# Performance work log

Hardware: AMD Instinct MI355X
Metric: run time of the kernel (lower is better)

The kernel has to match this reference:

```python
import jax, jax.numpy as jnp
import numpy as np

T, H, I, E, TOP_K = 2048, 1024, 768, 8, 2


def setup_inputs() -> dict:
    key = jax.random.key(0)
    kx, kg, ku, kd, kr = jax.random.split(key, 5)
    scale_h = 1.0 / np.sqrt(H)
    scale_i = 1.0 / np.sqrt(I)
    x = jax.random.normal(kx, (T, H), dtype=jnp.float32)
    gate_w = jax.random.normal(kg, (E, I, H), dtype=jnp.float32) * scale_h
    up_w = jax.random.normal(ku, (E, I, H), dtype=jnp.float32) * scale_h
    down_w = jax.random.normal(kd, (E, H, I), dtype=jnp.float32) * scale_i
    # Router: top-k over random logits, softmax over selected, scatter to dense [T, E]
    logits = jax.random.normal(kr, (T, E), dtype=jnp.float32)
    top_vals, top_idx = jax.lax.top_k(logits, TOP_K)          # [T, K]
    top_w = jax.nn.softmax(top_vals, axis=-1)                 # [T, K]
    rows = jnp.arange(T)[:, None]                             # [T, 1]
    masked_routing_weights = jnp.zeros((T, E), jnp.float32).at[rows, top_idx].set(top_w)
    expert_select_count = jnp.zeros((E,), jnp.int32).at[top_idx.reshape(-1)].add(1)
    return {
        "x": x,
        "gate_w": gate_w,
        "up_w": up_w,
        "down_w": down_w,
        "masked_routing_weights": masked_routing_weights,
        "expert_select_count": expert_select_count,
    }


def reference(x, gate_w, up_w, down_w, masked_routing_weights, expert_select_count):
    # custom_moe_glu: per-expert GLU MLP, combined with masked routing weights.
    # x: [T, H]; gate_w/up_w: [E, I, H]; down_w: [E, H, I]; routing: [T, E]
    g = jnp.einsum("th,eih->tei", x, gate_w)                  # [T, E, I]
    u = jnp.einsum("th,eih->tei", x, up_w)                    # [T, E, I]
    h = jax.nn.silu(g) * u                                    # fused GLU activation
    # down projection per expert, then weighted combine over experts
    out = jnp.einsum("tei,ehi,te->th", h, down_w, masked_routing_weights)
    return out
```

## Files before the change

### kernel.cpp

```cpp
#include <hip/hip_runtime.h>
#include <hip/hip_bf16.h>

#define T_TOK 2048
#define H_DIM 1024
#define I_DIM 768
#define NEXP  8
#define WPE   6291456

typedef short bf16x8  __attribute__((ext_vector_type(8)));
typedef short short4v __attribute__((ext_vector_type(4)));
typedef float f32x4   __attribute__((ext_vector_type(4)));

__device__ __forceinline__ short f2bf(float f) {
  __bf16 b = (__bf16)f;
  return __builtin_bit_cast(short, b);
}
__device__ __forceinline__ void gload16(const void* g, void* l) {
  __builtin_amdgcn_global_load_lds(
      (const __attribute__((address_space(1))) void*)g,
      (__attribute__((address_space(3))) void*)l, 16, 0, 0);
}
__device__ __forceinline__ int padcnt(int c) { return (c + 127) & ~127; }
__device__ __forceinline__ int ebase(const int* __restrict__ cnts, int e) {
  int b = 0;
#pragma unroll
  for (int i = 0; i < NEXP; ++i)
    if (i < e) b += padcnt(cnts[i]);
  return b;
}


__global__ __launch_bounds__(512) void compact_k(const float* __restrict__ routw,
                                                 int* __restrict__ wsI) {
  __shared__ int sc[8];
  int e = blockIdx.x, lane = threadIdx.x & 63, w = threadIdx.x >> 6;
  unsigned long long mk[4];
  int cnt = 0;
#pragma unroll
  for (int c = 0; c < 4; ++c) {
    int tk = w * 256 + c * 64 + lane;
    float v = routw[(size_t)tk * NEXP + e];
    mk[c] = __ballot(v > 0.f);
    cnt += __popcll(mk[c]);
  }
  if (lane == 0) sc[w] = cnt;
  __syncthreads();
  int run = 0;
#pragma unroll
  for (int j = 0; j < 8; ++j)
    if (j < w) run += sc[j];
#pragma unroll
  for (int c = 0; c < 4; ++c) {
    int tk = w * 256 + c * 64 + lane;
    if ((mk[c] >> lane) & 1ull) {
      int pos = __popcll(mk[c] & ((1ull << lane) - 1));
      wsI[64 + e * T_TOK + run + pos] = tk;
    }
    run += __popcll(mk[c]);
  }
  if (w == 7 && lane == 0) wsI[e] = run;
}

__global__ __launch_bounds__(256) void pre_k(const float* __restrict__ x,
                                             const float* __restrict__ gw,
                                             const float* __restrict__ uw,
                                             const float* __restrict__ dw,
                                             const int* __restrict__ wsI,
                                             unsigned short* __restrict__ xc,
                                             unsigned short* __restrict__ wbf,
                                             float* __restrict__ out) {
  int bid = blockIdx.x, tid = threadIdx.x;
  if (bid < 4096) {
    int e = bid >> 9, rb = bid & 511;
    int cnt = wsI[e];
    int pad = padcnt(cnt);
    int r = rb * 4 + (tid >> 6);
    if (r >= pad) return;
    int base = ebase(wsI, e);
    int col = (tid & 63) * 16;
    unsigned short* dst = xc + (size_t)(base + r) * H_DIM + col;
    if (r < cnt) {
      int tok = wsI[64 + e * T_TOK + r];
      const float* sr = x + (size_t)tok * H_DIM + col;
#pragma unroll
      for (int j = 0; j < 4; ++j) {
        float4 v = *(const float4*)(sr + j * 4);
        short4v b = {f2bf(v.x), f2bf(v.y), f2bf(v.z), f2bf(v.w)};
        *(short4v*)(dst + j * 4) = b;
      }
    } else {
#pragma unroll
      for (int j = 0; j < 4; ++j) {
        short4v z = {0, 0, 0, 0};
        *(short4v*)(dst + j * 4) = z;
      }
    }
  } else if (bid < 8704) {
    size_t off = ((size_t)(bid - 4096) * 256 + tid) * 16;
    int a = (int)(off / (size_t)WPE);
    size_t rem = off - (size_t)a * WPE;
    const float* s = ((a == 0) ? gw : (a == 1) ? uw : dw) + rem;
    unsigned short* o = wbf + (size_t)a * WPE + rem;
#pragma unroll
    for (int j = 0; j < 4; ++j) {
      float4 v = *(const float4*)(s + j * 4);
      short4v b = {f2bf(v.x), f2bf(v.y), f2bf(v.z), f2bf(v.w)};
      *(short4v*)(o + j * 4) = b;
    }
  } else {
    size_t off = ((size_t)(bid - 8704) * 256 + tid) * 16;
    f32x4 z = {0.f, 0.f, 0.f, 0.f};
#pragma unroll
    for (int j = 0; j < 4; ++j) *(f32x4*)(out + off + j * 4) = z;
  }
}

#define WB(v)                                              \
  do {                                                     \
    asm volatile("s_waitcnt vmcnt(" #v ")" ::: "memory");  \
    __builtin_amdgcn_s_barrier();                          \
    __builtin_amdgcn_sched_barrier(0);                     \
  } while (0)

__global__ __launch_bounds__(512, 2) void gemm1_k(
    const unsigned short* __restrict__ xc, const unsigned short* __restrict__ wbf,
    const int* __restrict__ wsI, unsigned short* __restrict__ h) {
  int e = blockIdx.x & 7, rr = blockIdx.x >> 3;
  int mt = rr & 15, nt = rr >> 4;
  int cnt = wsI[e];
  int m0 = mt * 128;
  if (m0 >= cnt) return;
  int base = ebase(wsI, e);
  int n0 = nt * 128;

  __shared__ unsigned short ls[5][12288];

  int tid = threadIdx.x, lane = tid & 63, w = tid >> 6;
  int wm = w >> 2, wn = w & 3;
  int fr = lane & 15, fg = lane >> 4;
  int srow = lane >> 2;
  int scol = (((lane & 3) ^ (srow & 3) ^ ((srow >> 2) & 1))) * 8;

  const unsigned short* srcA = xc + (size_t)(base + m0 + 16 * w + srow) * H_DIM + scol;
  const unsigned short* srcG = wbf + (size_t)(e * I_DIM + n0 + 16 * w + srow) * H_DIM + scol;
  const unsigned short* srcU = wbf + WPE + (size_t)(e * I_DIM + n0 + 16 * w + srow) * H_DIM + scol;

  int sl = ((fg ^ (fr & 3) ^ ((fr >> 2) & 1)) << 3);
  int roA[4], roB[4];
#pragma unroll
  for (int m = 0; m < 4; ++m) roA[m] = (wm * 64 + m * 16 + fr) * 32 + sl;
#pragma unroll
  for (int n = 0; n < 4; ++n) {
    int r2 = (n < 2) ? (wn * 32 + n * 16 + fr) : (128 + wn * 32 + (n - 2) * 16 + fr);
    roB[n] = 4096 + r2 * 32 + sl;
  }

  bf16x8 af[2][4], bv[2][4];
  f32x4 acc[4][4] = {};

#define STG1(hh)                                                     \
  do {                                                               \
    unsigned short* lb = &ls[(hh) % 5][0];                           \
    gload16(srcA + (hh) * 32, lb + w * 512);                         \
    gload16(srcG + (hh) * 32, lb + 4096 + w * 512);                  \
    gload16(srcU + (hh) * 32, lb + 4096 + (w + 8) * 512);            \
  } while (0)
#define LDF1(st, hh)                                                 \
  do {                                                               \
    const unsigned short* lb = &ls[(hh) % 5][0];                     \
    _Pragma("unroll") for (int m = 0; m < 4; ++m) af[st][m] = *(const bf16x8*)(lb + roA[m]); \
    _Pragma("unroll") for (int n = 0; n < 4; ++n) bv[st][n] = *(const bf16x8*)(lb + roB[n]); \
  } while (0)
#define MM1(st)                                                      \
  do {                                                               \
    __builtin_amdgcn_s_setprio(1);                                   \
    _Pragma("unroll") for (int m = 0; m < 4; ++m)                    \
      _Pragma("unroll") for (int n = 0; n < 4; ++n)                  \
        acc[m][n] = __builtin_amdgcn_mfma_f32_16x16x32_bf16(af[st][m], bv[st][n], acc[m][n], 0, 0, 0); \
    __builtin_amdgcn_s_setprio(0);                                   \
  } while (0)

  STG1(0); STG1(1); STG1(2); STG1(3);
  WB(6);
  LDF1(0, 0);
#pragma unroll
  for (int i = 0; i < 32; ++i) {
    if (i + 4 < 32) STG1(i + 4);
    if (i + 1 < 32) LDF1((i + 1) & 1, i + 1);
    MM1(i & 1);
    if (i <= 27)      WB(6);
    else if (i == 28) WB(3);
    else if (i == 29) WB(0);
  }
#undef STG1
#undef LDF1
#undef MM1

#pragma unroll
  for (int m = 0; m < 4; ++m)
#pragma unroll
    for (int j = 0; j < 4; ++j) {
      int row = wm * 64 + m * 16 + fg * 4 + j;
      size_t rb2 = (size_t)(base + m0 + row) * I_DIM + n0;
#pragma unroll
      for (int jn = 0; jn < 2; ++jn) {
        float g = acc[m][jn][j];
        float u = acc[m][jn + 2][j];
        h[rb2 + wn * 32 + jn * 16 + fr] = (unsigned short)f2bf(g * u / (1.f + __expf(-g)));
      }
    }
}

__global__ __launch_bounds__(512, 2) void gemm2_k(
    const unsigned short* __restrict__ h, const unsigned short* __restrict__ wbf,
    const int* __restrict__ wsI, const float* __restrict__ routw,
    float* __restrict__ out) {
  int e = blockIdx.x & 7, rr = blockIdx.x >> 3;
  int mt = rr & 15, nt = rr >> 4;
  int cnt = wsI[e];
  int m0 = mt * 128;
  if (m0 >= cnt) return;
  int base = ebase(wsI, e);
  int n0 = nt * 256;
  const unsigned short* down_bf = wbf + 2 * (size_t)WPE;

  __shared__ unsigned short ls[5][12288];

  int tid = threadIdx.x, lane = tid & 63, w = tid >> 6;
  int wm = w >> 2, wn = w & 3;
  int fr = lane & 15, fg = lane >> 4;
  int srow = lane >> 2;
  int scol = (((lane & 3) ^ (srow & 3) ^ ((srow >> 2) & 1))) * 8;

  const unsigned short* srcA  = h + (size_t)(base + m0 + 16 * w + srow) * I_DIM + scol;
  const unsigned short* srcB1 = down_bf + (size_t)(e * H_DIM + n0 + 16 * w + srow) * I_DIM + scol;
  const unsigned short* srcB2 = down_bf + (size_t)(e * H_DIM + n0 + 16 * (w + 8) + srow) * I_DIM + scol;

  int sl = ((fg ^ (fr & 3) ^ ((fr >> 2) & 1)) << 3);
  int roA[4], roB[4];
#pragma unroll
  for (int m = 0; m < 4; ++m) roA[m] = (wm * 64 + m * 16 + fr) * 32 + sl;
#pragma unroll
  for (int n = 0; n < 4; ++n) roB[n] = 4096 + (wn * 64 + n * 16 + fr) * 32 + sl;

  bf16x8 af[2][4], bv[2][4];
  f32x4 acc[4][4] = {};

#define STG2(hh)                                                     \
  do {                                                               \
    unsigned short* lb = &ls[(hh) % 5][0];                           \
    gload16(srcA + (hh) * 32, lb + w * 512);                         \
    gload16(srcB1 + (hh) * 32, lb + 4096 + w * 512);                 \
    gload16(srcB2 + (hh) * 32, lb + 4096 + (w + 8) * 512);           \
  } while (0)
#define LDF2(st, hh)                                                 \
  do {                                                               \
    const unsigned short* lb = &ls[(hh) % 5][0];                     \
    _Pragma("unroll") for (int m = 0; m < 4; ++m) af[st][m] = *(const bf16x8*)(lb + roA[m]); \
    _Pragma("unroll") for (int n = 0; n < 4; ++n) bv[st][n] = *(const bf16x8*)(lb + roB[n]); \
  } while (0)
#define MM2(st)                                                      \
  do {                                                               \
    __builtin_amdgcn_s_setprio(1);                                   \
    _Pragma("unroll") for (int m = 0; m < 4; ++m)                    \
      _Pragma("unroll") for (int n = 0; n < 4; ++n)                  \
        acc[m][n] = __builtin_amdgcn_mfma_f32_16x16x32_bf16(af[st][m], bv[st][n], acc[m][n], 0, 0, 0); \
    __builtin_amdgcn_s_setprio(0);                                   \
  } while (0)

  STG2(0); STG2(1); STG2(2); STG2(3);
  WB(6);
  LDF2(0, 0);
#pragma unroll
  for (int i = 0; i < 24; ++i) {
    if (i + 4 < 24) STG2(i + 4);
    if (i + 1 < 24) LDF2((i + 1) & 1, i + 1);
    MM2(i & 1);
    if (i <= 19)      WB(6);
    else if (i == 20) WB(3);
    else if (i == 21) WB(0);
  }
#undef STG2
#undef LDF2
#undef MM2

#pragma unroll
  for (int m = 0; m < 4; ++m)
#pragma unroll
    for (int j = 0; j < 4; ++j) {
      int row = wm * 64 + m * 16 + fg * 4 + j;
      int grow = m0 + row;
      if (grow < cnt) {
        int tk = wsI[64 + e * T_TOK + grow];
        float rw = routw[(size_t)tk * NEXP + e];
        float* orow = out + (size_t)tk * H_DIM + n0 + wn * 64;
#pragma unroll
        for (int n = 0; n < 4; ++n)
          atomicAdd(orow + n * 16 + fr, acc[m][n][j] * rw);
      }
    }
}

extern "C" void kernel_launch(void* const* d_in, const int* in_sizes, int n_in,
                              void* d_out, int out_size, void* d_ws, size_t ws_size,
                              hipStream_t stream) {
  const float* x      = (const float*)d_in[0];
  const float* gate_w = (const float*)d_in[1];
  const float* up_w   = (const float*)d_in[2];
  const float* down_w = (const float*)d_in[3];
  const float* routw  = (const float*)d_in[4];
  float* out = (float*)d_out;
  int* wsI = (int*)d_ws;

  unsigned short* wbf = (unsigned short*)((char*)d_ws + 131072);
  unsigned short* xc  = (unsigned short*)((char*)d_ws + 37879808);
  unsigned short* h   = (unsigned short*)((char*)d_ws + 48365568);

  compact_k<<<8, 512, 0, stream>>>(routw, wsI);
  pre_k<<<9216, 256, 0, stream>>>(x, gate_w, up_w, down_w, wsI, xc, wbf, out);
  gemm1_k<<<768, 512, 0, stream>>>(xc, wbf, wsI, h);
  gemm2_k<<<512, 512, 0, stream>>>(h, wbf, wsI, routw, out);
}
```

Before: 93.52 us.

## Rewrite gate/up GEMM to load fragments directly from global, exchanging up via LDS

The first grouped GEMM drops its 5-stage LDS pipeline with async global-to-LDS loads. It now uses 256-thread blocks over 64-row tiles, where each wave loads its MFMA operands straight from global memory into registers with double buffering. Gate and up products are computed by separate waves, and the up results pass through a small padded LDS buffer so the gate waves can apply SiLU and write h. The intent is to cut LDS traffic and barriers and raise occupancy. The cost is that A and B tiles are no longer shared across waves, so global and L2 traffic per MFMA rises, and the uncoalesced 16-byte row loads may limit bandwidth.

Measured after the change: 151.0 us. 61.5% more time.

```diff
diff --git a/kernel.cpp b/kernel.cpp
--- a/kernel.cpp
+++ b/kernel.cpp
@@ -115,101 +115,96 @@
   }
 }
 
+__global__ __launch_bounds__(256, 3) void gemm1_k(
+    const unsigned short* __restrict__ xc, const unsigned short* __restrict__ wbf,
+    const int* __restrict__ wsI, unsigned short* __restrict__ h) {
+  int e = blockIdx.x & 7, rr = blockIdx.x >> 3;
+  int mt = rr & 31, ng = rr >> 5;
+  int cnt = wsI[e];
+  int m0 = mt * 64;
+  if (m0 >= cnt) return;
+  int base = ebase(wsI, e);
+
+  __shared__ float uex[2][64][65];
+
+  int tid = threadIdx.x, lane = tid & 63, w = tid >> 6;
+  int fr = lane & 15, fg = lane >> 4;
+  int isU = w >> 1;
+  int wp = w & 1;
+  int n0 = ng * 128 + 64 * wp;
+
+  const unsigned short* wsrc = wbf + (size_t)isU * WPE;
+  const unsigned short* pa[4];
+  const unsigned short* pb[4];
+#pragma unroll
+  for (int m = 0; m < 4; ++m)
+    pa[m] = xc + (size_t)(base + m0 + m * 16 + fr) * H_DIM + fg * 8;
+#pragma unroll
+  for (int n = 0; n < 4; ++n)
+    pb[n] = wsrc + (size_t)(e * I_DIM + n0 + n * 16 + fr) * H_DIM + fg * 8;
+
+  f32x4 acc[4][4] = {};
+  bf16x8 a0[4], b0[4], a1[4], b1[4];
+
+#define LD1(A, B, ks)                                                \
+  do {                                                               \
+    _Pragma("unroll") for (int m = 0; m < 4; ++m)                    \
+      A[m] = *(const bf16x8*)(pa[m] + (ks) * 32);                    \
+    _Pragma("unroll") for (int n = 0; n < 4; ++n)                    \
+      B[n] = *(const bf16x8*)(pb[n] + (ks) * 32);                    \
+  } while (0)
+#define MM1(A, B)                                                    \
+  do {                                                               \
+    _Pragma("unroll") for (int m = 0; m < 4; ++m)                    \
+      _Pragma("unroll") for (int n = 0; n < 4; ++n)                  \
+        acc[m][n] = __builtin_amdgcn_mfma_f32_16x16x32_bf16(A[m], B[n], acc[m][n], 0, 0, 0); \
+  } while (0)
+
+  LD1(a0, b0, 0);
+  LD1(a1, b1, 1);
+#pragma unroll
+  for (int i = 0; i < 16; ++i) {
+    MM1(a0, b0);
+    if (i < 15) LD1(a0, b0, 2 * i + 2);
+    MM1(a1, b1);
+    if (i < 15) LD1(a1, b1, 2 * i + 3);
+  }
+#undef LD1
+#undef MM1
+
+  if (isU) {
+#pragma unroll
+    for (int m = 0; m < 4; ++m)
+#pragma unroll
+      for (int n = 0; n < 4; ++n)
+#pragma unroll
+        for (int j = 0; j < 4; ++j)
+          uex[wp][m * 16 + fg * 4 + j][n * 16 + fr] = acc[m][n][j];
+  }
+  __syncthreads();
+  if (!isU) {
+#pragma unroll
+    for (int m = 0; m < 4; ++m)
+#pragma unroll
+      for (int j = 0; j < 4; ++j) {
+        int row = m * 16 + fg * 4 + j;
+        size_t hb = (size_t)(base + m0 + row) * I_DIM + n0;
+#pragma unroll
+        for (int n = 0; n < 4; ++n) {
+          float g = acc[m][n][j];
+          float u = uex[wp][row][n * 16 + fr];
+          h[hb + n * 16 + fr] = (unsigned short)f2bf(g * u / (1.f + __expf(-g)));
+        }
+      }
+  }
+}
+
 #define WB(v)                                              \
   do {                                                     \
     asm volatile("s_waitcnt vmcnt(" #v ")" ::: "memory");  \
     __builtin_amdgcn_s_barrier();                          \
     __builtin_amdgcn_sched_barrier(0);                     \
   } while (0)
-
-__global__ __launch_bounds__(512, 2) void gemm1_k(
-    const unsigned short* __restrict__ xc, const unsigned short* __restrict__ wbf,
-    const int* __restrict__ wsI, unsigned short* __restrict__ h) {
-  int e = blockIdx.x & 7, rr = blockIdx.x >> 3;
-  int mt = rr & 15, nt = rr >> 4;
-  int cnt = wsI[e];
-  int m0 = mt * 128;
-  if (m0 >= cnt) return;
-  int base = ebase(wsI, e);
-  int n0 = nt * 128;
-
-  __shared__ unsigned short ls[5][12288];
-
-  int tid = threadIdx.x, lane = tid & 63, w = tid >> 6;
-  int wm = w >> 2, wn = w & 3;
-  int fr = lane & 15, fg = lane >> 4;
-  int srow = lane >> 2;
-  int scol = (((lane & 3) ^ (srow & 3) ^ ((srow >> 2) & 1))) * 8;
-
-  const unsigned short* srcA = xc + (size_t)(base + m0 + 16 * w + srow) * H_DIM + scol;
-  const unsigned short* srcG = wbf + (size_t)(e * I_DIM + n0 + 16 * w + srow) * H_DIM + scol;
-  const unsigned short* srcU = wbf + WPE + (size_t)(e * I_DIM + n0 + 16 * w + srow) * H_DIM + scol;
-
-  int sl = ((fg ^ (fr & 3) ^ ((fr >> 2) & 1)) << 3);
-  int roA[4], roB[4];
-#pragma unroll
-  for (int m = 0; m < 4; ++m) roA[m] = (wm * 64 + m * 16 + fr) * 32 + sl;
-#pragma unroll
-  for (int n = 0; n < 4; ++n) {
-    int r2 = (n < 2) ? (wn * 32 + n * 16 + fr) : (128 + wn * 32 + (n - 2) * 16 + fr);
-    roB[n] = 4096 + r2 * 32 + sl;
-  }
-
-  bf16x8 af[2][4], bv[2][4];
-  f32x4 acc[4][4] = {};
-
-#define STG1(hh)                                                     \
-  do {                                                               \
-    unsigned short* lb = &ls[(hh) % 5][0];                           \
-    gload16(srcA + (hh) * 32, lb + w * 512);                         \
-    gload16(srcG + (hh) * 32, lb + 4096 + w * 512);                  \
-    gload16(srcU + (hh) * 32, lb + 4096 + (w + 8) * 512);            \
-  } while (0)
-#define LDF1(st, hh)                                                 \
-  do {                                                               \
-    const unsigned short* lb = &ls[(hh) % 5][0];                     \
-    _Pragma("unroll") for (int m = 0; m < 4; ++m) af[st][m] = *(const bf16x8*)(lb + roA[m]); \
-    _Pragma("unroll") for (int n = 0; n < 4; ++n) bv[st][n] = *(const bf16x8*)(lb + roB[n]); \
-  } while (0)
-#define MM1(st)                                                      \
-  do {                                                               \
-    __builtin_amdgcn_s_setprio(1);                                   \
-    _Pragma("unroll") for (int m = 0; m < 4; ++m)                    \
-      _Pragma("unroll") for (int n = 0; n < 4; ++n)                  \
-        acc[m][n] = __builtin_amdgcn_mfma_f32_16x16x32_bf16(af[st][m], bv[st][n], acc[m][n], 0, 0, 0); \
-    __builtin_amdgcn_s_setprio(0);                                   \
-  } while (0)
-
-  STG1(0); STG1(1); STG1(2); STG1(3);
-  WB(6);
-  LDF1(0, 0);
-#pragma unroll
-  for (int i = 0; i < 32; ++i) {
-    if (i + 4 < 32) STG1(i + 4);
-    if (i + 1 < 32) LDF1((i + 1) & 1, i + 1);
-    MM1(i & 1);
-    if (i <= 27)      WB(6);
-    else if (i == 28) WB(3);
-    else if (i == 29) WB(0);
-  }
-#undef STG1
-#undef LDF1
-#undef MM1
-
-#pragma unroll
-  for (int m = 0; m < 4; ++m)
-#pragma unroll
-    for (int j = 0; j < 4; ++j) {
-      int row = wm * 64 + m * 16 + fg * 4 + j;
-      size_t rb2 = (size_t)(base + m0 + row) * I_DIM + n0;
-#pragma unroll
-      for (int jn = 0; jn < 2; ++jn) {
-        float g = acc[m][jn][j];
-        float u = acc[m][jn + 2][j];
-        h[rb2 + wn * 32 + jn * 16 + fr] = (unsigned short)f2bf(g * u / (1.f + __expf(-g)));
-      }
-    }
-}
 
 __global__ __launch_bounds__(512, 2) void gemm2_k(
     const unsigned short* __restrict__ h, const unsigned short* __restrict__ wbf,
@@ -318,6 +313,6 @@
 
   compact_k<<<8, 512, 0, stream>>>(routw, wsI);
   pre_k<<<9216, 256, 0, stream>>>(x, gate_w, up_w, down_w, wsI, xc, wbf, out);
-  gemm1_k<<<768, 512, 0, stream>>>(xc, wbf, wsI, h);
+  gemm1_k<<<1536, 256, 0, stream>>>(xc, wbf, wsI, h);
   gemm2_k<<<512, 512, 0, stream>>>(h, wbf, wsI, routw, out);
 }
```

## Gather tokens inside gemm1 from padded bf16 x instead of precompacted copy

Applied to the files above, without the earlier changes.

Instead of building a per-expert compacted bf16 copy of x in the prep kernel, x is converted once into a bf16 buffer with an extra zero row, and gemm1 gathers rows by token index, with padding indices pointing at the zero row. The x and gate/up weight buffers also get a padded row stride of 1056 elements, likely to spread accesses across memory channels. This cuts prep-kernel traffic, since x is converted once rather than per expert assignment. The cost is an indirect, non-contiguous row load for the A operand in gemm1.

Result: faster. 91.60 us (-2.0%).

```diff
diff --git a/kernel.cpp b/kernel.cpp
--- a/kernel.cpp
+++ b/kernel.cpp
@@ -5,7 +5,8 @@
 #define H_DIM 1024
 #define I_DIM 768
 #define NEXP  8
-#define WPE   6291456
+#define XSTR  1056
+#define WSTR  1056
 
 typedef short bf16x8  __attribute__((ext_vector_type(8)));
 typedef short short4v __attribute__((ext_vector_type(4)));
@@ -33,7 +34,7 @@
 __global__ __launch_bounds__(512) void compact_k(const float* __restrict__ routw,
                                                  int* __restrict__ wsI) {
   __shared__ int sc[8];
-  int e = blockIdx.x, lane = threadIdx.x & 63, w = threadIdx.x >> 6;
+  int e = blockIdx.x, tid = threadIdx.x, lane = tid & 63, w = tid >> 6;
   unsigned long long mk[4];
   int cnt = 0;
 #pragma unroll
@@ -45,10 +46,12 @@
   }
   if (lane == 0) sc[w] = cnt;
   __syncthreads();
-  int run = 0;
-#pragma unroll
-  for (int j = 0; j < 8; ++j)
+  int run = 0, tot = 0;
+#pragma unroll
+  for (int j = 0; j < 8; ++j) {
     if (j < w) run += sc[j];
+    tot += sc[j];
+  }
 #pragma unroll
   for (int c = 0; c < 4; ++c) {
     int tk = w * 256 + c * 64 + lane;
@@ -58,30 +61,28 @@
     }
     run += __popcll(mk[c]);
   }
-  if (w == 7 && lane == 0) wsI[e] = run;
+  if (w == 7 && lane == 0) wsI[e] = tot;
+  int pad = padcnt(tot);
+  for (int r = tot + tid; r < pad; r += 512) wsI[64 + e * T_TOK + r] = T_TOK;
 }
 
 __global__ __launch_bounds__(256) void pre_k(const float* __restrict__ x,
                                              const float* __restrict__ gw,
                                              const float* __restrict__ uw,
                                              const float* __restrict__ dw,
-                                             const int* __restrict__ wsI,
-                                             unsigned short* __restrict__ xc,
-                                             unsigned short* __restrict__ wbf,
+                                             unsigned short* __restrict__ x_bf,
+                                             unsigned short* __restrict__ gbf,
+                                             unsigned short* __restrict__ ubf,
+                                             unsigned short* __restrict__ dbf,
                                              float* __restrict__ out) {
   int bid = blockIdx.x, tid = threadIdx.x;
-  if (bid < 4096) {
-    int e = bid >> 9, rb = bid & 511;
-    int cnt = wsI[e];
-    int pad = padcnt(cnt);
-    int r = rb * 4 + (tid >> 6);
-    if (r >= pad) return;
-    int base = ebase(wsI, e);
-    int col = (tid & 63) * 16;
-    unsigned short* dst = xc + (size_t)(base + r) * H_DIM + col;
-    if (r < cnt) {
-      int tok = wsI[64 + e * T_TOK + r];
-      const float* sr = x + (size_t)tok * H_DIM + col;
+  int col = (tid & 63) * 16;
+  if (bid < 520) {
+    int r = bid * 4 + (tid >> 6);
+    if (r > 2048) return;
+    unsigned short* dst = x_bf + (size_t)r * XSTR + col;
+    if (r < 2048) {
+      const float* sr = x + (size_t)r * H_DIM + col;
 #pragma unroll
       for (int j = 0; j < 4; ++j) {
         float4 v = *(const float4*)(sr + j * 4);
@@ -95,12 +96,21 @@
         *(short4v*)(dst + j * 4) = z;
       }
     }
-  } else if (bid < 8704) {
-    size_t off = ((size_t)(bid - 4096) * 256 + tid) * 16;
-    int a = (int)(off / (size_t)WPE);
-    size_t rem = off - (size_t)a * WPE;
-    const float* s = ((a == 0) ? gw : (a == 1) ? uw : dw) + rem;
-    unsigned short* o = wbf + (size_t)a * WPE + rem;
+  } else if (bid < 3592) {
+    int a = (bid < 2056) ? 0 : 1;
+    int r = (bid - (a ? 2056 : 520)) * 4 + (tid >> 6);
+    const float* s = (a ? uw : gw) + (size_t)r * H_DIM + col;
+    unsigned short* dst = (a ? ubf : gbf) + (size_t)r * WSTR + col;
+#pragma unroll
+    for (int j = 0; j < 4; ++j) {
+      float4 v = *(const float4*)(s + j * 4);
+      short4v b = {f2bf(v.x), f2bf(v.y), f2bf(v.z), f2bf(v.w)};
+      *(short4v*)(dst + j * 4) = b;
+    }
+  } else if (bid < 5128) {
+    size_t off = ((size_t)(bid - 3592) * 256 + tid) * 16;
+    const float* s = dw + off;
+    unsigned short* o = dbf + off;
 #pragma unroll
     for (int j = 0; j < 4; ++j) {
       float4 v = *(const float4*)(s + j * 4);
@@ -108,7 +118,7 @@
       *(short4v*)(o + j * 4) = b;
     }
   } else {
-    size_t off = ((size_t)(bid - 8704) * 256 + tid) * 16;
+    size_t off = ((size_t)(bid - 5128) * 256 + tid) * 16;
     f32x4 z = {0.f, 0.f, 0.f, 0.f};
 #pragma unroll
     for (int j = 0; j < 4; ++j) *(f32x4*)(out + off + j * 4) = z;
@@ -123,8 +133,9 @@
   } while (0)
 
 __global__ __launch_bounds__(512, 2) void gemm1_k(
-    const unsigned short* __restrict__ xc, const unsigned short* __restrict__ wbf,
-    const int* __restrict__ wsI, unsigned short* __restrict__ h) {
+    const unsigned short* __restrict__ x_bf, const unsigned short* __restrict__ gbf,
+    const unsigned short* __restrict__ ubf, const int* __restrict__ wsI,
+    unsigned short* __restrict__ h) {
   int e = blockIdx.x & 7, rr = blockIdx.x >> 3;
   int mt = rr & 15, nt = rr >> 4;
   int cnt = wsI[e];
@@ -141,9 +152,10 @@
   int srow = lane >> 2;
   int scol = (((lane & 3) ^ (srow & 3) ^ ((srow >> 2) & 1))) * 8;
 
-  const unsigned short* srcA = xc + (size_t)(base + m0 + 16 * w + srow) * H_DIM + scol;
-  const unsigned short* srcG = wbf + (size_t)(e * I_DIM + n0 + 16 * w + srow) * H_DIM + scol;
-  const unsigned short* srcU = wbf + WPE + (size_t)(e * I_DIM + n0 + 16 * w + srow) * H_DIM + scol;
+  int tokA = wsI[64 + e * T_TOK + m0 + 16 * w + srow];
+  const unsigned short* srcA = x_bf + (size_t)tokA * XSTR + scol;
+  const unsigned short* srcG = gbf + (size_t)(e * I_DIM + n0 + 16 * w + srow) * WSTR + scol;
+  const unsigned short* srcU = ubf + (size_t)(e * I_DIM + n0 + 16 * w + srow) * WSTR + scol;
 
   int sl = ((fg ^ (fr & 3) ^ ((fr >> 2) & 1)) << 3);
   int roA[4], roB[4];
@@ -212,7 +224,7 @@
 }
 
 __global__ __launch_bounds__(512, 2) void gemm2_k(
-    const unsigned short* __restrict__ h, const unsigned short* __restrict__ wbf,
+    const unsigned short* __restrict__ h, const unsigned short* __restrict__ dbf,
     const int* __restrict__ wsI, const float* __restrict__ routw,
     float* __restrict__ out) {
   int e = blockIdx.x & 7, rr = blockIdx.x >> 3;
@@ -222,7 +234,6 @@
   if (m0 >= cnt) return;
   int base = ebase(wsI, e);
   int n0 = nt * 256;
-  const unsigned short* down_bf = wbf + 2 * (size_t)WPE;
 
   __shared__ unsigned short ls[5][12288];
 
@@ -233,8 +244,8 @@
   int scol = (((lane & 3) ^ (srow & 3) ^ ((srow >> 2) & 1))) * 8;
 
   const unsigned short* srcA  = h + (size_t)(base + m0 + 16 * w + srow) * I_DIM + scol;
-  const unsigned short* srcB1 = down_bf + (size_t)(e * H_DIM + n0 + 16 * w + srow) * I_DIM + scol;
-  const unsigned short* srcB2 = down_bf + (size_t)(e * H_DIM + n0 + 16 * (w + 8) + srow) * I_DIM + scol;
+  const unsigned short* srcB1 = dbf + (size_t)(e * H_DIM + n0 + 16 * w + srow) * I_DIM + scol;
+  const unsigned short* srcB2 = dbf + (size_t)(e * H_DIM + n0 + 16 * (w + 8) + srow) * I_DIM + scol;
 
   int sl = ((fg ^ (fr & 3) ^ ((fr >> 2) & 1)) << 3);
   int roA[4], roB[4];
@@ -312,12 +323,14 @@
   float* out = (float*)d_out;
   int* wsI = (int*)d_ws;
 
-  unsigned short* wbf = (unsigned short*)((char*)d_ws + 131072);
-  unsigned short* xc  = (unsigned short*)((char*)d_ws + 37879808);
-  unsigned short* h   = (unsigned short*)((char*)d_ws + 48365568);
+  unsigned short* x_bf = (unsigned short*)((char*)d_ws + 131072);
+  unsigned short* gbf  = (unsigned short*)((char*)d_ws + 4458560);
+  unsigned short* ubf  = (unsigned short*)((char*)d_ws + 17434688);
+  unsigned short* dbf  = (unsigned short*)((char*)d_ws + 30410816);
+  unsigned short* h    = (unsigned short*)((char*)d_ws + 42993728);
 
   compact_k<<<8, 512, 0, stream>>>(routw, wsI);
-  pre_k<<<9216, 256, 0, stream>>>(x, gate_w, up_w, down_w, wsI, xc, wbf, out);
-  gemm1_k<<<768, 512, 0, stream>>>(xc, wbf, wsI, h);
-  gemm2_k<<<512, 512, 0, stream>>>(h, wbf, wsI, routw, out);
-}
+  pre_k<<<5640, 256, 0, stream>>>(x, gate_w, up_w, down_w, x_bf, gbf, ubf, dbf, out);
+  gemm1_k<<<768, 512, 0, stream>>>(x_bf, gbf, ubf, wsI, h);
+  gemm2_k<<<512, 512, 0, stream>>>(h, dbf, wsI, routw, out);
+}
```
